# Kernel tuning notes

Measured on AMD Instinct MI355X. Metric: run time of the kernel, lower is better.

Reference implementation:

```python
import jax, jax.numpy as jnp
import numpy as np


def setup_inputs() -> dict:
    key = jax.random.key(0)
    k1, k2 = jax.random.split(key)
    N, M, D = 16384, 4096, 512
    input = jax.random.normal(k1, (N, D), dtype=jnp.float32)
    centres = jax.random.normal(k2, (M, D), dtype=jnp.float32)
    return {"input": input, "centres": centres}


def reference(input, centres):
    # Mathematically identical to (x - c).pow(2).sum(-1) without the
    # O(N*M*D) expanded intermediate.
    x_sq = jnp.sum(input * input, axis=-1, keepdims=True)        # [N, 1]
    c_sq = jnp.sum(centres * centres, axis=-1)[None, :]          # [1, M]
    cross = jnp.einsum("nd,md->nm", input, centres)             # [N, M]
    return x_sq + c_sq - 2.0 * cross                             # [N, M]
```

## Files before the change

### kernel.cpp

```cpp
#include <hip/hip_runtime.h>
#include <hip/hip_bf16.h>
#include <stdint.h>

#define N_ROWS 16384
#define M_ROWS 4096
#define DDIM   512

using frag_ab = __attribute__((ext_vector_type(8))) short;
using frag_cd = __attribute__((ext_vector_type(4))) float;

__device__ __forceinline__ unsigned short f2bf(float f) {
  unsigned int u = __float_as_uint(f);
  u += 0x7fffu + ((u >> 16) & 1u);
  return (unsigned short)(u >> 16);
}

__global__ void rbf_convert_kernel(const float* __restrict__ in,
                                   const float* __restrict__ cen,
                                   unsigned short* __restrict__ a_bf,
                                   unsigned short* __restrict__ b_bf,
                                   float* __restrict__ x_sq,
                                   float* __restrict__ c_sq) {
  const int wave = threadIdx.x >> 6;
  const int lane = threadIdx.x & 63;
  const int row  = blockIdx.x * 4 + wave;

  const float* src;
  unsigned short* dst;
  float* nrm;
  if (row < N_ROWS) {
    src = in + (long)row * DDIM;
    dst = a_bf + (long)row * DDIM;
    nrm = x_sq + row;
  } else {
    const int rr = row - N_ROWS;
    src = cen + (long)rr * DDIM;
    dst = b_bf + (long)rr * DDIM;
    nrm = c_sq + rr;
  }

  float sum = 0.f;
#pragma unroll
  for (int it = 0; it < 2; ++it) {
    const int col = it * 256 + lane * 4;
    float4 v = *(const float4*)(src + col);
    sum += v.x * v.x + v.y * v.y + v.z * v.z + v.w * v.w;
    ushort4 p;
    p.x = f2bf(v.x); p.y = f2bf(v.y); p.z = f2bf(v.z); p.w = f2bf(v.w);
    *(ushort4*)(dst + col) = p;
  }
#pragma unroll
  for (int off = 32; off > 0; off >>= 1) sum += __shfl_down(sum, off, 64);
  if (lane == 0) *nrm = sum;
}

__global__ __launch_bounds__(256) void rbf_gemm_kernel(
    const unsigned short* __restrict__ a_bf,
    const unsigned short* __restrict__ b_bf,
    const float* __restrict__ x_sq,
    const float* __restrict__ c_sq,
    float* __restrict__ out) {
  __shared__ __attribute__((aligned(16))) unsigned short A_lds[128 * 32];
  __shared__ __attribute__((aligned(16))) unsigned short B_lds[128 * 32];

  const int tid    = threadIdx.x;
  const int wave   = tid >> 6;
  const int lane   = tid & 63;
  const int lane15 = lane & 15;
  const int quad   = lane >> 4;
  const int wr     = wave >> 1;
  const int wc     = wave & 1;
  const int n0     = blockIdx.y * 128;
  const int m0     = blockIdx.x * 128;

  frag_cd acc[4][4];
#pragma unroll
  for (int i = 0; i < 4; ++i)
#pragma unroll
    for (int j = 0; j < 4; ++j)
      acc[i][j] = (frag_cd){0.f, 0.f, 0.f, 0.f};

  for (int kb = 0; kb < DDIM / 32; ++kb) {
    const int k0 = kb * 32;
#pragma unroll
    for (int it = 0; it < 2; ++it) {
      const int cbase = (it * 4 + wave) * 64;
      const int c     = cbase + lane;
      const int row   = c >> 2;
      const int kc    = c & 3;
      const unsigned short* ga = a_bf + (long)(n0 + row) * DDIM + k0 + kc * 8;
      const unsigned short* gb = b_bf + (long)(m0 + row) * DDIM + k0 + kc * 8;
      __builtin_amdgcn_global_load_lds(
          (const __attribute__((address_space(1))) unsigned int*)ga,
          (__attribute__((address_space(3))) unsigned int*)&A_lds[cbase * 8],
          16, 0, 0);
      __builtin_amdgcn_global_load_lds(
          (const __attribute__((address_space(1))) unsigned int*)gb,
          (__attribute__((address_space(3))) unsigned int*)&B_lds[cbase * 8],
          16, 0, 0);
    }
    __syncthreads();

    frag_ab a_frag[4], b_frag[4];
#pragma unroll
    for (int i = 0; i < 4; ++i) {
      const int r = wr * 64 + i * 16 + lane15;
      a_frag[i] = *(const frag_ab*)&A_lds[r * 32 + quad * 8];
    }
#pragma unroll
    for (int j = 0; j < 4; ++j) {
      const int r = wc * 64 + j * 16 + lane15;
      b_frag[j] = *(const frag_ab*)&B_lds[r * 32 + quad * 8];
    }
#pragma unroll
    for (int i = 0; i < 4; ++i)
#pragma unroll
      for (int j = 0; j < 4; ++j)
        acc[i][j] = __builtin_amdgcn_mfma_f32_16x16x32_bf16(
            a_frag[i], b_frag[j], acc[i][j], 0, 0, 0);
    __syncthreads();
  }

  float cs[4];
#pragma unroll
  for (int j = 0; j < 4; ++j) cs[j] = c_sq[m0 + wc * 64 + j * 16 + lane15];

#pragma unroll
  for (int i = 0; i < 4; ++i) {
#pragma unroll
    for (int reg = 0; reg < 4; ++reg) {
      const int r = n0 + wr * 64 + i * 16 + quad * 4 + reg;
      const float xv = x_sq[r];
      float* orow = out + (long)r * M_ROWS + m0 + wc * 64 + lane15;
#pragma unroll
      for (int j = 0; j < 4; ++j) {
        orow[j * 16] = xv + cs[j] - 2.0f * acc[i][j][reg];
      }
    }
  }
}

extern "C" void kernel_launch(void* const* d_in, const int* in_sizes, int n_in,
                              void* d_out, int out_size, void* d_ws, size_t ws_size,
                              hipStream_t stream) {
  const float* input   = (const float*)d_in[0];
  const float* centres = (const float*)d_in[1];
  float* out = (float*)d_out;

  char* ws = (char*)d_ws;
  unsigned short* a_bf = (unsigned short*)ws;
  unsigned short* b_bf = (unsigned short*)(ws + (size_t)N_ROWS * DDIM * 2);
  float* x_sq = (float*)(ws + (size_t)N_ROWS * DDIM * 2 + (size_t)M_ROWS * DDIM * 2);
  float* c_sq = x_sq + N_ROWS;

  rbf_convert_kernel<<<(N_ROWS + M_ROWS) / 4, 256, 0, stream>>>(
      input, centres, a_bf, b_bf, x_sq, c_sq);

  dim3 grid(M_ROWS / 128, N_ROWS / 128);
  rbf_gemm_kernel<<<grid, 256, 0, stream>>>(a_bf, b_bf, x_sq, c_sq, out);
}
```

Baseline: 357.3 us.

## Rewrite GEMM with 256x256 tiles, 4-stage LDS pipeline, swizzle and XCD remap

The GEMM kernel is restructured to use 512-thread blocks computing 256x256 output tiles. A/B tiles are staged through a 4-slot LDS ring buffer with three tiles in flight, using explicit vmcnt waits in place of two full syncthreads per k-step. LDS addresses are XOR-swizzled to avoid bank conflicts, workgroup IDs are remapped across XCDs for L2 locality, MFMA priority is raised, and output stores become nontemporal. The cost is more LDS (128KB) and more register pressure, which limits occupancy.

```diff
diff --git a/kernel.cpp b/kernel.cpp
--- a/kernel.cpp
+++ b/kernel.cpp
@@ -5,6 +5,8 @@
 #define N_ROWS 16384
 #define M_ROWS 4096
 #define DDIM   512
+#define BK     32
+#define NKT    (DDIM / BK)
 
 using frag_ab = __attribute__((ext_vector_type(8))) short;
 using frag_cd = __attribute__((ext_vector_type(4))) float;
@@ -54,87 +56,124 @@
   if (lane == 0) *nrm = sum;
 }
 
-__global__ __launch_bounds__(256) void rbf_gemm_kernel(
+__global__ __launch_bounds__(512, 2) void rbf_gemm_kernel(
     const unsigned short* __restrict__ a_bf,
     const unsigned short* __restrict__ b_bf,
     const float* __restrict__ x_sq,
     const float* __restrict__ c_sq,
     float* __restrict__ out) {
-  __shared__ __attribute__((aligned(16))) unsigned short A_lds[128 * 32];
-  __shared__ __attribute__((aligned(16))) unsigned short B_lds[128 * 32];
+  __shared__ __attribute__((aligned(16))) unsigned short A_lds[4][256 * BK];
+  __shared__ __attribute__((aligned(16))) unsigned short B_lds[4][256 * BK];
 
   const int tid    = threadIdx.x;
-  const int wave   = tid >> 6;
+  const int wid    = tid >> 6;
   const int lane   = tid & 63;
   const int lane15 = lane & 15;
   const int quad   = lane >> 4;
-  const int wr     = wave >> 1;
-  const int wc     = wave & 1;
-  const int n0     = blockIdx.y * 128;
-  const int m0     = blockIdx.x * 128;
-
-  frag_cd acc[4][4];
-#pragma unroll
-  for (int i = 0; i < 4; ++i)
+  const int wm     = wid >> 2;
+  const int wn     = wid & 3;
+
+  const int orig = blockIdx.x;
+  const int wg   = (orig & 7) * 128 + (orig >> 3);
+  const int m0   = (wg & 15) * 256;
+  const int n0   = (wg >> 4) * 256;
+
+  const unsigned short* srcA[2];
+  const unsigned short* srcB[2];
+  int dstc[2];
+#pragma unroll
+  for (int it = 0; it < 2; ++it) {
+    const int o   = (it * 512 + tid) * 16;
+    const int op  = o ^ ((o >> 3) & 48);
+    const int row = op >> 6;
+    const int ke  = (op & 63) >> 1;
+    srcA[it] = a_bf + (size_t)(n0 + row) * DDIM + ke;
+    srcB[it] = b_bf + (size_t)(m0 + row) * DDIM + ke;
+    dstc[it] = (it * 512 + tid) * 8;
+  }
+
+  int offA[8], offB[4];
+#pragma unroll
+  for (int i = 0; i < 8; ++i) {
+    const int row = wm * 128 + i * 16 + lane15;
+    const int L   = row * 64 + quad * 16;
+    offA[i] = L ^ ((L >> 3) & 48);
+  }
+#pragma unroll
+  for (int j = 0; j < 4; ++j) {
+    const int row = wn * 64 + j * 16 + lane15;
+    const int L   = row * 64 + quad * 16;
+    offB[j] = L ^ ((L >> 3) & 48);
+  }
+
+  frag_cd acc[8][4];
+#pragma unroll
+  for (int i = 0; i < 8; ++i)
 #pragma unroll
     for (int j = 0; j < 4; ++j)
       acc[i][j] = (frag_cd){0.f, 0.f, 0.f, 0.f};
 
-  for (int kb = 0; kb < DDIM / 32; ++kb) {
-    const int k0 = kb * 32;
+  auto stage = [&](int slot, int kt) {
 #pragma unroll
     for (int it = 0; it < 2; ++it) {
-      const int cbase = (it * 4 + wave) * 64;
-      const int c     = cbase + lane;
-      const int row   = c >> 2;
-      const int kc    = c & 3;
-      const unsigned short* ga = a_bf + (long)(n0 + row) * DDIM + k0 + kc * 8;
-      const unsigned short* gb = b_bf + (long)(m0 + row) * DDIM + k0 + kc * 8;
       __builtin_amdgcn_global_load_lds(
-          (const __attribute__((address_space(1))) unsigned int*)ga,
-          (__attribute__((address_space(3))) unsigned int*)&A_lds[cbase * 8],
+          (const __attribute__((address_space(1))) unsigned int*)(srcA[it] + kt * BK),
+          (__attribute__((address_space(3))) unsigned int*)&A_lds[slot][dstc[it]],
           16, 0, 0);
       __builtin_amdgcn_global_load_lds(
-          (const __attribute__((address_space(1))) unsigned int*)gb,
-          (__attribute__((address_space(3))) unsigned int*)&B_lds[cbase * 8],
+          (const __attribute__((address_space(1))) unsigned int*)(srcB[it] + kt * BK),
+          (__attribute__((address_space(3))) unsigned int*)&B_lds[slot][dstc[it]],
           16, 0, 0);
     }
-    __syncthreads();
-
-    frag_ab a_frag[4], b_frag[4];
-#pragma unroll
-    for (int i = 0; i < 4; ++i) {
-      const int r = wr * 64 + i * 16 + lane15;
-      a_frag[i] = *(const frag_ab*)&A_lds[r * 32 + quad * 8];
-    }
-#pragma unroll
-    for (int j = 0; j < 4; ++j) {
-      const int r = wc * 64 + j * 16 + lane15;
-      b_frag[j] = *(const frag_ab*)&B_lds[r * 32 + quad * 8];
-    }
-#pragma unroll
-    for (int i = 0; i < 4; ++i)
+  };
+
+  stage(0, 0);
+  stage(1, 1);
+  stage(2, 2);
+
+#pragma unroll
+  for (int kt = 0; kt < NKT; ++kt) {
+    if (kt <= NKT - 3)      asm volatile("s_waitcnt vmcnt(8)" ::: "memory");
+    else if (kt == NKT - 2) asm volatile("s_waitcnt vmcnt(4)" ::: "memory");
+    else                    asm volatile("s_waitcnt vmcnt(0)" ::: "memory");
+    __builtin_amdgcn_s_barrier();
+    __builtin_amdgcn_sched_barrier(0);
+
+    if (kt + 3 < NKT) stage((kt + 3) & 3, kt + 3);
+
+    const char* Ab = (const char*)&A_lds[kt & 3][0];
+    const char* Bb = (const char*)&B_lds[kt & 3][0];
+    frag_ab a[8], b[4];
+#pragma unroll
+    for (int j = 0; j < 4; ++j) b[j] = *(const frag_ab*)(Bb + offB[j]);
+#pragma unroll
+    for (int i = 0; i < 8; ++i) a[i] = *(const frag_ab*)(Ab + offA[i]);
+
+    __builtin_amdgcn_s_setprio(1);
+#pragma unroll
+    for (int i = 0; i < 8; ++i)
 #pragma unroll
       for (int j = 0; j < 4; ++j)
         acc[i][j] = __builtin_amdgcn_mfma_f32_16x16x32_bf16(
-            a_frag[i], b_frag[j], acc[i][j], 0, 0, 0);
-    __syncthreads();
+            a[i], b[j], acc[i][j], 0, 0, 0);
+    __builtin_amdgcn_s_setprio(0);
   }
 
   float cs[4];
 #pragma unroll
-  for (int j = 0; j < 4; ++j) cs[j] = c_sq[m0 + wc * 64 + j * 16 + lane15];
-
-#pragma unroll
-  for (int i = 0; i < 4; ++i) {
+  for (int j = 0; j < 4; ++j) cs[j] = c_sq[m0 + wn * 64 + j * 16 + lane15];
+
+#pragma unroll
+  for (int i = 0; i < 8; ++i) {
 #pragma unroll
     for (int reg = 0; reg < 4; ++reg) {
-      const int r = n0 + wr * 64 + i * 16 + quad * 4 + reg;
+      const int r = n0 + wm * 128 + i * 16 + quad * 4 + reg;
       const float xv = x_sq[r];
-      float* orow = out + (long)r * M_ROWS + m0 + wc * 64 + lane15;
+      float* orow = out + (size_t)r * M_ROWS + m0 + wn * 64 + lane15;
 #pragma unroll
       for (int j = 0; j < 4; ++j) {
-        orow[j * 16] = xv + cs[j] - 2.0f * acc[i][j][reg];
+        __builtin_nontemporal_store(xv + cs[j] - 2.0f * acc[i][j][reg],
+                                    orow + j * 16);
       }
     }
   }
@@ -156,6 +195,6 @@
   rbf_convert_kernel<<<(N_ROWS + M_ROWS) / 4, 256, 0, stream>>>(
       input, centres, a_bf, b_bf, x_sq, c_sq);
 
-  dim3 grid(M_ROWS / 128, N_ROWS / 128);
-  rbf_gemm_kernel<<<grid, 256, 0, stream>>>(a_bf, b_bf, x_sq, c_sq, out);
-}
+  rbf_gemm_kernel<<<(N_ROWS / 256) * (M_ROWS / 256), 512, 0, stream>>>(
+      a_bf, b_bf, x_sq, c_sq, out);
+}
```

Result: no change. 359.1 us (+0.5%).
